# Optimization experiments

Hardware: AMD Instinct MI355X
Metric: run time of the kernel (lower is better)

The kernel has to match this reference:

```python
import jax, jax.numpy as jnp
import numpy as np

NMS_RADIUS = 2.0   # cfgs.NMS_radius (meters)
EPS = 1e-6         # torch nn.PairwiseDistance default eps (added to the diff)
M = 16384          # number of keypoint candidates
SCENE = 100.0      # scene extent in meters


def setup_inputs() -> dict:
    key = jax.random.key(0)
    k1, k2 = jax.random.split(key)
    nodes = jax.random.uniform(k1, (M, 3), dtype=jnp.float32) * SCENE
    overlap_score = jax.random.normal(k2, (M,), dtype=jnp.float32)
    return {"nodes": nodes, "overlap_score": overlap_score}


def _greedy_nms(nodes, radius):
    """Sequential greedy NMS: keep node i iff its distance to every
    already-kept node exceeds radius. Faithful to the torch loop:
    (dis > radius).sum() == n_kept  <=>  all kept dists > radius."""
    n = nodes.shape[0]

    def body(i, mask):
        # torch nn.PairwiseDistance computes ||x1 - x2 + eps||_2
        d = jnp.linalg.norm(nodes[i] - nodes + EPS, axis=-1)  # [n]
        keep = jnp.all(jnp.where(mask, d > radius, True))
        return mask.at[i].set(keep)

    mask0 = jnp.zeros(n, dtype=bool).at[0].set(True)
    return jax.lax.fori_loop(1, n, body, mask0)


def reference(nodes, overlap_score):
    # sort by overlap score descending, run greedy NMS, unsort the mask
    order = jnp.argsort(-overlap_score)
    mask_sorted = _greedy_nms(nodes[order], NMS_RADIUS)
    mask = jnp.zeros_like(mask_sorted).at[order].set(mask_sorted)
    nms_length = mask.sum(dtype=jnp.int32)[None]
    return mask, nms_length
```

## Files before the change

kernel.cpp:

```cpp
#include <hip/hip_runtime.h>


#define M_PTS    16384
#define RADIUS   2.0f
#define EPS_D    1e-6f
#define GRID_N   25
#define NCELLS   (GRID_N * GRID_N * GRID_N)
#define CELL_CAP 12
#define K_NBR    12
#define ACT_CAP  4608


__device__ __forceinline__ int cell_of(float v) {
  int c = (int)(v * 0.25f);
  return c < 0 ? 0 : (c > GRID_N - 1 ? GRID_N - 1 : c);
}

__global__ __launch_bounds__(256) void grid_build(
    const float* __restrict__ nodes, const float* __restrict__ score,
    float4* __restrict__ pts, int* __restrict__ cell_cnt,
    unsigned short* __restrict__ cell_list) {
  int i = blockIdx.x * 256 + threadIdx.x;
  if (i >= M_PTS) return;
  float4 p;
  p.x = nodes[3 * i + 0];
  p.y = nodes[3 * i + 1];
  p.z = nodes[3 * i + 2];
  p.w = score[i];
  pts[i] = p;
  int cid = (cell_of(p.x) * GRID_N + cell_of(p.y)) * GRID_N + cell_of(p.z);
  int pos = atomicAdd(&cell_cnt[cid], 1);
  if (pos < CELL_CAP) cell_list[cid * CELL_CAP + pos] = (unsigned short)i;
}

__global__ __launch_bounds__(256) void nbr_scan(
    const float4* __restrict__ pts, const int* __restrict__ cell_cnt,
    const unsigned short* __restrict__ cell_list,
    int* __restrict__ cnt, unsigned short* __restrict__ nbr) {
  int t = blockIdx.x * 256 + threadIdx.x;
  int i = t / 27;
  int d = t - i * 27;
  if (i >= M_PTS) return;
  const float4 pi = pts[i];
  int cx = cell_of(pi.x) + (d / 9) - 1;
  int cy = cell_of(pi.y) + ((d / 3) % 3) - 1;
  int cz = cell_of(pi.z) + (d % 3) - 1;
  if (cx < 0 || cx >= GRID_N || cy < 0 || cy >= GRID_N ||
      cz < 0 || cz >= GRID_N) return;
  int cid = (cx * GRID_N + cy) * GRID_N + cz;
  int m = cell_cnt[cid];
  if (m > CELL_CAP) m = CELL_CAP;
  for (int s = 0; s < m; ++s) {
    int j = cell_list[cid * CELL_CAP + s];
    float4 pj = pts[j];
    bool earlier = (pj.w > pi.w) || ((pj.w == pi.w) && (j < i));
    if (!earlier) continue;
    float ddx = __fadd_rn(__fsub_rn(pi.x, pj.x), EPS_D);
    float ddy = __fadd_rn(__fsub_rn(pi.y, pj.y), EPS_D);
    float ddz = __fadd_rn(__fsub_rn(pi.z, pj.z), EPS_D);
    float d2 = __fadd_rn(__fadd_rn(__fmul_rn(ddx, ddx), __fmul_rn(ddy, ddy)),
                         __fmul_rn(ddz, ddz));
    float dist = __fsqrt_rn(d2);
    if (!(dist > RADIUS)) {
      int pos = atomicAdd(&cnt[i], 1);
      if (pos < K_NBR) nbr[i * K_NBR + pos] = (unsigned short)j;
    }
  }
}

__global__ __launch_bounds__(1024) void solve_kernel(
    const int* __restrict__ cnt, const unsigned short* __restrict__ nbr,
    int* __restrict__ out, int out_size) {
  __shared__ unsigned char mask[M_PTS];
  __shared__ unsigned int nbr_s[ACT_CAP][6];
  __shared__ unsigned int act[ACT_CAP];
  __shared__ int act_n, changed, total;

  const int tid = threadIdx.x;
  if (tid == 0) { act_n = 0; total = 0; }
  __syncthreads();

  for (int k = tid; k < M_PTS; k += 1024) {
    mask[k] = 1;
    int c = cnt[k];
    if (c > K_NBR) c = K_NBR;
    if (c > 0) {
      int pos = atomicAdd(&act_n, 1);
      if (pos < ACT_CAP) act[pos] = (unsigned)k | ((unsigned)c << 16);
    }
  }
  __syncthreads();
  const int na_raw = act_n;
  const bool ok = (na_raw <= ACT_CAP);
  const int na = ok ? na_raw : ACT_CAP;

  if (ok) {
    for (int a = tid; a < na; a += 1024) {
      int k = (int)(act[a] & 0xFFFFu);
      const unsigned int* src = (const unsigned int*)(nbr + (size_t)k * K_NBR);
#pragma unroll
      for (int w = 0; w < 6; ++w) nbr_s[a][w] = src[w];
    }
  }
  __syncthreads();

  for (int it = 0; it < 512; ++it) {
    if (tid == 0) changed = 0;
    __syncthreads();
    int any = 0;
    if (ok) {
      for (int a = tid; a < na; a += 1024) {
        unsigned e = act[a];
        int k = (int)(e & 0xFFFFu);
        int c = (int)(e >> 16);
        const unsigned short* row = (const unsigned short*)nbr_s[a];
        int kp = 1;
        for (int t = 0; t < c; ++t) kp &= (int)(mask[row[t]] ^ 1);
        if (kp != (int)mask[k]) { mask[k] = (unsigned char)kp; any = 1; }
      }
    } else {
      for (int k = tid; k < M_PTS; k += 1024) {
        int c = cnt[k]; if (c > K_NBR) c = K_NBR;
        if (!c) continue;
        int kp = 1;
        for (int t = 0; t < c; ++t) kp &= (int)(mask[nbr[k * K_NBR + t]] ^ 1);
        if (kp != (int)mask[k]) { mask[k] = (unsigned char)kp; any = 1; }
      }
    }
    if (any) changed = 1;
    __syncthreads();
    if (!changed) break;
  }

  int ks = 0;
  for (int k = tid; k < M_PTS; k += 1024) {
    int m = (int)mask[k];
    out[k] = m;
    ks += m;
  }
#pragma unroll
  for (int off = 32; off > 0; off >>= 1) ks += __shfl_down(ks, off, 64);
  if ((tid & 63) == 0) atomicAdd(&total, ks);
  __syncthreads();
  if (tid == 0) out[out_size - 1] = total;
}

extern "C" void kernel_launch(void* const* d_in, const int* in_sizes, int n_in,
                              void* d_out, int out_size, void* d_ws, size_t ws_size,
                              hipStream_t stream) {
  const float* nodes = (const float*)d_in[0];
  const float* score = (const float*)d_in[1];
  int* out = (int*)d_out;

  char* ws = (char*)d_ws;
  float4* pts = (float4*)ws;
  int* cell_cnt = (int*)(ws + 262144);
  int* cnt = (int*)(ws + 324644);
  unsigned short* cell_list = (unsigned short*)(ws + 393216);
  unsigned short* nbr = (unsigned short*)(ws + 770048);

  hipMemsetAsync(ws + 262144, 0, 62500 + 65536, stream);
  grid_build<<<64, 256, 0, stream>>>(nodes, score, pts, cell_cnt, cell_list);
  nbr_scan<<<1728, 256, 0, stream>>>(pts, cell_cnt, cell_list, cnt, nbr);
  solve_kernel<<<1, 1024, 0, stream>>>(cnt, nbr, out, out_size);
}
```

Before: 41.32 us.

## Run asynchronous relaxation sweeps between barriers and replace memset with zero kernel

The fixed-point solve now does four unsynchronized sweeps over a volatile shared mask, then a checked sweep with __syncthreads_count, instead of a barrier and shared flag every iteration. This cuts block-wide synchronization per convergence step and lets updates propagate within a sweep in chaotic-relaxation style. The hipMemsetAsync is replaced by a small zero kernel to avoid memset launch overhead. Convergence to the same greedy result relies on the monotone dependency structure, and races on the mask are tolerated by design.

```diff
diff --git a/kernel.cpp b/kernel.cpp
--- a/kernel.cpp
+++ b/kernel.cpp
@@ -14,6 +14,11 @@
 __device__ __forceinline__ int cell_of(float v) {
   int c = (int)(v * 0.25f);
   return c < 0 ? 0 : (c > GRID_N - 1 ? GRID_N - 1 : c);
+}
+
+__global__ __launch_bounds__(256) void zero_kernel(int4* __restrict__ p) {
+  int i = blockIdx.x * 256 + threadIdx.x;
+  if (i < 8003) p[i] = make_int4(0, 0, 0, 0);
 }
 
 __global__ __launch_bounds__(256) void grid_build(
@@ -71,17 +76,18 @@
 __global__ __launch_bounds__(1024) void solve_kernel(
     const int* __restrict__ cnt, const unsigned short* __restrict__ nbr,
     int* __restrict__ out, int out_size) {
-  __shared__ unsigned char mask[M_PTS];
+  __shared__ unsigned char mask_[M_PTS];
   __shared__ unsigned int nbr_s[ACT_CAP][6];
   __shared__ unsigned int act[ACT_CAP];
-  __shared__ int act_n, changed, total;
+  __shared__ int act_n, total;
+  volatile unsigned char* mask = mask_;
 
   const int tid = threadIdx.x;
   if (tid == 0) { act_n = 0; total = 0; }
   __syncthreads();
 
   for (int k = tid; k < M_PTS; k += 1024) {
-    mask[k] = 1;
+    mask_[k] = 1;
     int c = cnt[k];
     if (c > K_NBR) c = K_NBR;
     if (c > 0) {
@@ -104,11 +110,21 @@
   }
   __syncthreads();
 
-  for (int it = 0; it < 512; ++it) {
-    if (tid == 0) changed = 0;
-    __syncthreads();
-    int any = 0;
-    if (ok) {
+  if (ok) {
+    for (int grp = 0; grp < 128; ++grp) {
+      for (int g = 0; g < 4; ++g) {
+        for (int a = tid; a < na; a += 1024) {
+          unsigned e = act[a];
+          int k = (int)(e & 0xFFFFu);
+          int c = (int)(e >> 16);
+          const unsigned short* row = (const unsigned short*)nbr_s[a];
+          int kp = 1;
+          for (int t = 0; t < c; ++t) kp &= (int)(mask[row[t]] ^ 1);
+          if (kp != (int)mask[k]) mask[k] = (unsigned char)kp;
+        }
+        asm volatile("" ::: "memory");
+      }
+      int any = 0;
       for (int a = tid; a < na; a += 1024) {
         unsigned e = act[a];
         int k = (int)(e & 0xFFFFu);
@@ -118,23 +134,31 @@
         for (int t = 0; t < c; ++t) kp &= (int)(mask[row[t]] ^ 1);
         if (kp != (int)mask[k]) { mask[k] = (unsigned char)kp; any = 1; }
       }
-    } else {
+      if (__syncthreads_count(any) == 0) break;
+    }
+  } else {
+    __shared__ int changed;
+    for (int it = 0; it < 512; ++it) {
+      if (tid == 0) changed = 0;
+      __syncthreads();
+      int any = 0;
       for (int k = tid; k < M_PTS; k += 1024) {
         int c = cnt[k]; if (c > K_NBR) c = K_NBR;
         if (!c) continue;
         int kp = 1;
         for (int t = 0; t < c; ++t) kp &= (int)(mask[nbr[k * K_NBR + t]] ^ 1);
-        if (kp != (int)mask[k]) { mask[k] = (unsigned char)kp; any = 1; }
+        if (kp != (int)mask[k]) { mask_[k] = (unsigned char)kp; any = 1; }
       }
+      if (any) changed = 1;
+      __syncthreads();
+      if (!changed) break;
     }
-    if (any) changed = 1;
-    __syncthreads();
-    if (!changed) break;
   }
+  __syncthreads();
 
   int ks = 0;
   for (int k = tid; k < M_PTS; k += 1024) {
-    int m = (int)mask[k];
+    int m = (int)mask_[k];
     out[k] = m;
     ks += m;
   }
@@ -159,7 +183,7 @@
   unsigned short* cell_list = (unsigned short*)(ws + 393216);
   unsigned short* nbr = (unsigned short*)(ws + 770048);
 
-  hipMemsetAsync(ws + 262144, 0, 62500 + 65536, stream);
+  zero_kernel<<<32, 256, 0, stream>>>((int4*)(ws + 262144));
   grid_build<<<64, 256, 0, stream>>>(nodes, score, pts, cell_cnt, cell_list);
   nbr_scan<<<1728, 256, 0, stream>>>(pts, cell_cnt, cell_list, cnt, nbr);
   solve_kernel<<<1, 1024, 0, stream>>>(cnt, nbr, out, out_size);
```

Measured after the change: 40.88 us. Within noise of the previous version (-1.1%).
